# Kernel tuning notes

Measured on AMD Instinct MI355X. Metric: run time of the kernel, lower is better.

Reference implementation:

```python
import jax, jax.numpy as jnp
import numpy as np

HD = 36      # hard-coded per-head dim in the module
TOPK = 16
EPS = 1e-6


def _adaln(h, emb, w, b):
    # w: (2*D, E) torch-layout Linear weight, b: (2*D,)
    eo = jax.nn.silu(emb) @ w.T + b            # (B, 2D)
    scale, shift = jnp.split(eo, 2, axis=-1)   # (B, D) each
    mu = jnp.mean(h, axis=-1, keepdims=True)
    var = jnp.var(h, axis=-1, keepdims=True)   # biased var, matches torch LayerNorm
    hn = (h - mu) / jnp.sqrt(var + EPS)
    return hn * (1.0 + scale[:, None]) + shift[:, None]


def setup_inputs() -> dict:
    B, T, D, E, N, H = 4, 512, 512, 512, 4096, 8
    key = jax.random.key(0)
    ks = jax.random.split(key, 18)
    s = 0.02
    f32 = jnp.float32
    return {
        "x1": jax.random.normal(ks[0], (B, T, D), f32),
        "x2": jax.random.normal(ks[1], (B, T, D), f32),
        "x3": jax.random.normal(ks[2], (B, T, D), f32),
        "xf": jax.random.normal(ks[3], (B, N, D), f32),
        "emb": jax.random.normal(ks[4], (B, E), f32),
        "u_noise": jax.random.uniform(ks[5], (B, H, 3 * T, N // H), f32),
        # AdaLN modulation Linear per branch (zero-init in source; use small random to exercise math)
        "adaln_w": jax.random.normal(ks[6], (3, 2 * D, E), f32) * s,
        "adaln_b": jnp.zeros((3, 2 * D), f32),
        "xfn_w": jax.random.normal(ks[7], (2 * D, E), f32) * s,
        "xfn_b": jnp.zeros((2 * D,), f32),
        "q_w": jax.random.normal(ks[8], (3, H * HD, D), f32) * s,
        "q_b": jnp.zeros((3, H * HD), f32),
        "k_w": jax.random.normal(ks[9], (H, HD, D), f32) * s,
        "k_b": jnp.zeros((H, HD), f32),
        "v_w": jax.random.normal(ks[10], (H, HD, D), f32) * s,
        "v_b": jnp.zeros((H, HD), f32),
        "out_w": jax.random.normal(ks[11], (3, D, H * HD), f32) * s,
        "out_b": jnp.zeros((3, D), f32),
    }


def reference(x1, x2, x3, xf, emb, u_noise, adaln_w, adaln_b, xfn_w, xfn_b,
              q_w, q_b, k_w, k_b, v_w, v_b, out_w, out_b):
    B = x1.shape[0]
    H = k_w.shape[0]
    N = xf.shape[1]
    nh = N // H
    Ts = (x1.shape[1], x2.shape[1], x3.shape[1])

    Qs = []
    for i, x in enumerate((x1, x2, x3)):
        xn = _adaln(x, emb, adaln_w[i], adaln_b[i])
        q = xn @ q_w[i].T + q_b[i]                               # (B,Ti,H*HD)
        Qs.append(q.reshape(B, x.shape[1], H, HD).transpose(0, 2, 1, 3))
    Q = jnp.concatenate(Qs, axis=2)                               # (B,H,T,HD)

    xfn = _adaln(xf, emb, xfn_w, xfn_b).reshape(B, H, nh, -1)     # (B,H,nh,D)
    K = jnp.einsum('bhnd,hkd->bhnk', xfn, k_w) + k_b[:, None, :]  # (B,H,nh,HD)
    V = jnp.einsum('bhnd,hkd->bhnk', xfn, v_w) + v_b[:, None, :]

    logits = jnp.einsum('bhtk,bhnk->bhtn', Q, K) / jnp.sqrt(jnp.float32(HD))
    gumbel = -jnp.log(-jnp.log(u_noise + 1e-9) + 1e-9)
    logits = logits + gumbel                                      # (B,H,T,nh)

    soft = jax.nn.softmax(logits, axis=-1)
    idx = jax.lax.top_k(logits, TOPK)[1]                          # (B,H,T,K)
    mask = jnp.put_along_axis(jnp.zeros_like(logits), idx, 1.0, axis=-1, inplace=False)
    hard = jax.nn.softmax(jnp.where(mask == 0, -jnp.inf, logits), axis=-1)
    attn = hard + soft - jax.lax.stop_gradient(soft)              # straight-through

    out = jnp.einsum('bhtn,bhnk->bhtk', attn, V)                  # (B,H,T,HD)
    out = out.transpose(0, 2, 1, 3).reshape(B, sum(Ts), H * HD)

    o1 = out[:, :Ts[0]] @ out_w[0].T + out_b[0]
    o2 = out[:, Ts[0]:Ts[0] + Ts[1]] @ out_w[1].T + out_b[1]
    o3 = out[:, Ts[0] + Ts[1]:] @ out_w[2].T + out_b[2]
    return (o1, o2, o3)
```

## Files before the change

### kernel.cpp

```cpp
#include <hip/hip_runtime.h>
#include <math.h>

#define FI4(p) (*(const float4*)(p))

typedef _Float16 half8 __attribute__((ext_vector_type(8)));
typedef _Float16 half2v __attribute__((ext_vector_type(2)));
typedef float f32x4 __attribute__((ext_vector_type(4)));

__device__ __forceinline__ float gumbelf(float u) {
    return -__logf(-__logf(u + 1e-9f) + 1e-9f);
}

template<int CTRL>
__device__ __forceinline__ int dppmov(int v) {
    return __builtin_amdgcn_update_dpp(v, v, CTRL, 0xF, 0xF, false);
}
__device__ __forceinline__ float wave_max_bcast(float v) {
    v = fmaxf(v, __int_as_float(dppmov<0xB1>(__float_as_int(v))));
    v = fmaxf(v, __int_as_float(dppmov<0x4E>(__float_as_int(v))));
    v = fmaxf(v, __int_as_float(dppmov<0x141>(__float_as_int(v))));
    v = fmaxf(v, __int_as_float(dppmov<0x140>(__float_as_int(v))));
    v = fmaxf(v, __int_as_float(dppmov<0x142>(__float_as_int(v))));
    v = fmaxf(v, __int_as_float(dppmov<0x143>(__float_as_int(v))));
    return __int_as_float(__builtin_amdgcn_readlane(__float_as_int(v), 63));
}
__device__ __forceinline__ float wave_sum_bcast(float v) {
    v += __int_as_float(dppmov<0xB1>(__float_as_int(v)));
    v += __int_as_float(dppmov<0x4E>(__float_as_int(v)));
    v += __int_as_float(dppmov<0x141>(__float_as_int(v)));
    v += __int_as_float(dppmov<0x140>(__float_as_int(v)));
    v += __int_as_float(dppmov<0x142>(__float_as_int(v)));
    v += __int_as_float(dppmov<0x143>(__float_as_int(v)));
    return __int_as_float(__builtin_amdgcn_readlane(__float_as_int(v), 63));
}

__device__ __forceinline__ unsigned ordkey(float f) {
    unsigned x = __float_as_uint(f);
    return x ^ ((unsigned)((int)x >> 31) | 0x80000000u);
}

__device__ __forceinline__ int mbcnt64(unsigned long long m) {
    return __builtin_amdgcn_mbcnt_hi((unsigned)(m >> 32),
           __builtin_amdgcn_mbcnt_lo((unsigned)m, 0));
}

__device__ __forceinline__ void copy8(unsigned long long* dst, const unsigned long long* src) {
    #pragma unroll
    for (int j = 0; j < 8; ++j) dst[j] = src[j];
}

__device__ __forceinline__ void tie_fill(const unsigned* u, unsigned long long* sel, unsigned hi)
{
    unsigned long long eq[8];
    int mcnt = 0;
    #pragma unroll
    for (int j = 0; j < 8; ++j) {
        sel[j] = __ballot(u[j] > hi);
        eq[j]  = __ballot(u[j] == hi);
        mcnt += __popcll(sel[j]);
    }
    int r = 16 - mcnt;
    #pragma unroll
    for (int jhi = 0; jhi < 2; ++jhi) {
        if (r > 0) {
            unsigned long long any = eq[jhi*4] | eq[jhi*4+1] | eq[jhi*4+2] | eq[jhi*4+3];
            while (any && r > 0) {
                int lane = (int)__builtin_ctzll(any); any &= any - 1;
                #pragma unroll
                for (int jlo = 0; jlo < 4; ++jlo) {
                    int j2 = jhi * 4 + jlo;
                    if (r > 0 && ((eq[j2] >> lane) & 1ull)) { sel[j2] |= 1ull << lane; --r; }
                }
            }
        }
    }
}

__device__ __forceinline__ void select16_pair(
    const unsigned* uA, const unsigned* uB,
    unsigned long long* selA, unsigned long long* selB,
    unsigned loA, unsigned hiA, unsigned loB, unsigned hiB)
{
    bool doneA = false, doneB = false;
    {
        unsigned long long mmA[8], mmB[8];
        int cA = 0, cB = 0;
        #pragma unroll
        for (int j = 0; j < 8; ++j) {
            mmA[j] = __ballot(uA[j] > loA); cA += __popcll(mmA[j]);
            mmB[j] = __ballot(uB[j] > loB); cB += __popcll(mmB[j]);
        }
        if (cA == 16) { copy8(selA, mmA); doneA = true; }
        else if (cA < 16) loA = 0u;
        if (cB == 16) { copy8(selB, mmB); doneB = true; }
        else if (cB < 16) loB = 0u;
    }
    while ((!doneA && hiA - loA > 1u) || (!doneB && hiB - loB > 1u)) {
        bool pA = !doneA && (hiA - loA > 1u);
        bool pB = !doneB && (hiB - loB > 1u);
        unsigned midA = loA + ((hiA - loA) >> 1);
        unsigned midB = loB + ((hiB - loB) >> 1);
        unsigned long long mmA[8], mmB[8];
        int cA = 0, cB = 0;
        #pragma unroll
        for (int j = 0; j < 8; ++j) {
            mmA[j] = __ballot(uA[j] > midA); cA += __popcll(mmA[j]);
            mmB[j] = __ballot(uB[j] > midB); cB += __popcll(mmB[j]);
        }
        if (pA) {
            if (cA == 16) { copy8(selA, mmA); doneA = true; }
            else if (cA > 16) loA = midA; else hiA = midA;
        }
        if (pB) {
            if (cB == 16) { copy8(selB, mmB); doneB = true; }
            else if (cB > 16) loB = midB; else hiB = midB;
        }
    }
    if (!doneA) tie_fill(uA, selA, hiA);
    if (!doneB) tie_fill(uB, selB, hiB);
}

__global__ __launch_bounds__(256) void prep_kernel(
    const float* __restrict__ q_w, const float* __restrict__ k_w,
    const float* __restrict__ v_w, const float* __restrict__ out_w,
    const float* __restrict__ emb,
    const float* __restrict__ adaln_w, const float* __restrict__ adaln_b,
    const float* __restrict__ xfn_w,  const float* __restrict__ xfn_b,
    _Float16* __restrict__ qwh, _Float16* __restrict__ qwl,
    _Float16* __restrict__ kwh, _Float16* __restrict__ kwl,
    _Float16* __restrict__ vw16, _Float16* __restrict__ ow16,
    float* __restrict__ eo)
{
    if (blockIdx.x < 4608) {
        int idx = blockIdx.x * 256 + threadIdx.x;
        if (idx < 442368) {
            float x = q_w[idx];
            _Float16 hi = (_Float16)x;
            qwh[idx] = hi; qwl[idx] = (_Float16)(x - (float)hi);
        } else if (idx < 442368 + 147456) {
            int i = idx - 442368;
            float x = k_w[i];
            _Float16 hi = (_Float16)x;
            kwh[i] = hi; kwl[i] = (_Float16)(x - (float)hi);
        } else if (idx < 442368 + 294912) {
            int i = idx - 442368 - 147456;
            vw16[i] = (_Float16)v_w[i];
        } else {
            int i = idx - 442368 - 294912;
            ow16[i] = (_Float16)out_w[i];
        }
    } else {
        int wid  = (blockIdx.x - 4608) * 4 + (threadIdx.x >> 6);
        int lane = threadIdx.x & 63;
        int l = wid >> 12;
        int rem = wid & 4095;
        int b = rem >> 10;
        int o = rem & 1023;
        const float* wrow = (l < 3) ? (adaln_w + ((size_t)(l * 1024 + o)) * 512)
                                    : (xfn_w + (size_t)o * 512);
        const float* erow = emb + b * 512;
        float acc = 0.f;
        for (int d = lane; d < 512; d += 64) {
            float e = erow[d];
            float se = e / (1.f + __expf(-e));
            acc = fmaf(se, wrow[d], acc);
        }
        #pragma unroll
        for (int off = 32; off; off >>= 1) acc += __shfl_xor(acc, off, 64);
        if (lane == 0) {
            float bias = (l < 3) ? adaln_b[l * 1024 + o] : xfn_b[o];
            eo[wid] = acc + bias;
        }
    }
}

__global__ __launch_bounds__(256) void ln_kernel(
    const float* __restrict__ x1, const float* __restrict__ x2,
    const float* __restrict__ x3, const float* __restrict__ xf,
    const float* __restrict__ eo,
    _Float16* __restrict__ xnqh, _Float16* __restrict__ xnql,
    _Float16* __restrict__ xfnh, _Float16* __restrict__ xfnl)
{
    int row = blockIdx.x;
    const float* src; const float* eorow; _Float16* dh; _Float16* dl;
    if (row < 6144) {
        int l = row >> 11, idx = row & 2047, b = idx >> 9;
        const float* xp = (l == 0) ? x1 : (l == 1) ? x2 : x3;
        src = xp + (size_t)idx * 512;
        eorow = eo + (size_t)(l * 4 + b) * 1024;
        dh = xnqh + (size_t)row * 512;
        dl = xnql + (size_t)row * 512;
    } else {
        int rr = row - 6144; int b = rr >> 12;
        src = xf + (size_t)rr * 512;
        eorow = eo + (size_t)(12 + b) * 1024;
        dh = xfnh + (size_t)rr * 512;
        dl = xfnl + (size_t)rr * 512;
    }
    int tid = threadIdx.x;
    float2 vv = *(const float2*)(src + 2 * tid);
    float s = vv.x + vv.y;
    float q = fmaf(vv.x, vv.x, vv.y * vv.y);
    #pragma unroll
    for (int off = 32; off; off >>= 1) {
        s += __shfl_xor(s, off, 64);
        q += __shfl_xor(q, off, 64);
    }
    __shared__ float red[8];
    int wv = tid >> 6, lane = tid & 63;
    if (lane == 0) { red[wv] = s; red[4 + wv] = q; }
    __syncthreads();
    s = red[0] + red[1] + red[2] + red[3];
    q = red[4] + red[5] + red[6] + red[7];
    float mu  = s * (1.f / 512.f);
    float var = q * (1.f / 512.f) - mu * mu;
    float rs  = 1.f / sqrtf(var + 1e-6f);
    float2 sc = *(const float2*)(eorow + 2 * tid);
    float2 sh = *(const float2*)(eorow + 512 + 2 * tid);
    float r0 = (vv.x - mu) * rs * (1.f + sc.x) + sh.x;
    float r1 = (vv.y - mu) * rs * (1.f + sc.y) + sh.y;
    _Float16 h0 = (_Float16)r0, h1 = (_Float16)r1;
    half2v H = {h0, h1};
    half2v L = {(_Float16)(r0 - (float)h0), (_Float16)(r1 - (float)h1)};
    *(half2v*)(dh + 2 * tid) = H;
    *(half2v*)(dl + 2 * tid) = L;
}

template<int NF, int MODE>
__device__ __forceinline__ void gemm16_body(
    int gw, int l,
    const _Float16* __restrict__ Ah, const _Float16* __restrict__ Al,
    const _Float16* __restrict__ Wh, const _Float16* __restrict__ Wl,
    const float* __restrict__ bias,
    float* __restrict__ O0)
{
    constexpr bool SPLIT = (MODE == 0 || MODE == 1);
    const int Kd = (MODE == 3) ? 288 : 512;
    const int NT = (MODE == 0) ? 6 : (MODE == 3) ? 8 : 1;
    const int mt = gw / NT, nt = gw - mt * NT;
    const int row0 = mt * 32;
    const int col0 = nt * (NF * 16);
    const int lr = l & 15, lk = (l >> 4) * 8;

    int lsel = 0, h = 0;
    if (MODE == 0)                   { lsel = row0 >> 11; }
    else if (MODE == 1 || MODE == 2) { h = (row0 >> 9) & 7; }
    else                             { lsel = row0 >> 11; }

    size_t arow0;
    if (MODE == 3) {
        int rb = row0 & 2047, bb = rb >> 9, t0 = rb & 511;
        arow0 = (size_t)bb * 1536 + (size_t)lsel * 512 + t0;
    } else {
        arow0 = (size_t)row0;
    }

    const _Float16* aph = Ah + (arow0 + lr) * Kd + lk;
    const _Float16* apl = SPLIT ? (Al + (arow0 + lr) * Kd + lk) : nullptr;

    const _Float16* bph[NF];
    const _Float16* bpl[NF];
    #pragma unroll
    for (int f = 0; f < NF; ++f) {
        int c = col0 + f * 16 + lr;
        int wr;
        if (MODE == 0)      wr = lsel * 288 + c;
        else if (MODE == 3) wr = lsel * 512 + c;
        else                wr = h * 36 + (c < 36 ? c : 0);
        bph[f] = Wh + (size_t)wr * Kd + lk;
        if (SPLIT) bpl[f] = Wl + (size_t)wr * Kd + lk;
    }

    f32x4 acc[2][NF];
    #pragma unroll
    for (int mi = 0; mi < 2; ++mi)
        #pragma unroll
        for (int f = 0; f < NF; ++f) acc[mi][f] = (f32x4){0.f, 0.f, 0.f, 0.f};

    for (int kk = 0; kk < Kd; kk += 32) {
        half8 a0h = *(const half8*)(aph + kk);
        half8 a1h = *(const half8*)(aph + (size_t)16 * Kd + kk);
        half8 a0l, a1l;
        if constexpr (SPLIT) {
            a0l = *(const half8*)(apl + kk);
            a1l = *(const half8*)(apl + (size_t)16 * Kd + kk);
        }
        #pragma unroll
        for (int f = 0; f < NF; ++f) {
            half8 bh_ = *(const half8*)(bph[f] + kk);
            acc[0][f] = __builtin_amdgcn_mfma_f32_16x16x32_f16(a0h, bh_, acc[0][f], 0, 0, 0);
            acc[1][f] = __builtin_amdgcn_mfma_f32_16x16x32_f16(a1h, bh_, acc[1][f], 0, 0, 0);
            if constexpr (SPLIT) {
                half8 bl_ = *(const half8*)(bpl[f] + kk);
                acc[0][f] = __builtin_amdgcn_mfma_f32_16x16x32_f16(a0h, bl_, acc[0][f], 0, 0, 0);
                acc[1][f] = __builtin_amdgcn_mfma_f32_16x16x32_f16(a1h, bl_, acc[1][f], 0, 0, 0);
                acc[0][f] = __builtin_amdgcn_mfma_f32_16x16x32_f16(a0l, bh_, acc[0][f], 0, 0, 0);
                acc[1][f] = __builtin_amdgcn_mfma_f32_16x16x32_f16(a1l, bh_, acc[1][f], 0, 0, 0);
            }
        }
    }

    #pragma unroll
    for (int mi = 0; mi < 2; ++mi) {
        int rbase = row0 + mi * 16 + (l >> 4) * 4;
        #pragma unroll
        for (int f = 0; f < NF; ++f) {
            int c = col0 + f * 16 + (l & 15);
            if (MODE == 0) {
                int hh = c / 36, hd = c - hh * 36;
                float bz = bias[lsel * 288 + c];
                #pragma unroll
                for (int j = 0; j < 4; ++j) {
                    int r = rbase + j;
                    int rb = r & 2047, bb2 = rb >> 9, t = rb & 511;
                    O0[(((size_t)bb2 * 8 + hh) * 1536 + lsel * 512 + t) * 36 + hd]
                        = acc[mi][f][j] + bz;
                }
            } else if (MODE == 1) {
                if (c < 36) {
                    int bb2 = row0 >> 12;
                    int n0 = rbase & 511;
                    float bz = bias[h * 36 + c];
                    float4 v4;
                    v4.x = acc[mi][f][0] + bz; v4.y = acc[mi][f][1] + bz;
                    v4.z = acc[mi][f][2] + bz; v4.w = acc[mi][f][3] + bz;
                    *(float4*)&O0[(((size_t)bb2 * 8 + h) * 36 + c) * 512 + n0] = v4;
                }
            } else if (MODE == 2) {
                if (c < 36) {
                    int bb2 = row0 >> 12;
                    int n0 = rbase & 511;
                    float bz = bias[h * 36 + c];
                    #pragma unroll
                    for (int j = 0; j < 4; ++j)
                        O0[(((size_t)bb2 * 8 + h) * 512 + n0 + j) * 36 + c]
                            = acc[mi][f][j] + bz;
                }
            } else {
                float bz = bias[lsel * 512 + c];
                #pragma unroll
                for (int j = 0; j < 4; ++j) {
                    int r = rbase + j;
                    int rb = r & 2047, bb2 = rb >> 9, t = rb & 511;
                    O0[(size_t)lsel * 1048576 + ((size_t)bb2 * 512 + t) * 512 + c]
                        = acc[mi][f][j] + bz;
                }
            }
        }
    }
}

__global__ __launch_bounds__(256) void qkv_kernel(
    const _Float16* __restrict__ xnqh, const _Float16* __restrict__ xnql,
    const _Float16* __restrict__ xfnh, const _Float16* __restrict__ xfnl,
    const _Float16* __restrict__ qwh,  const _Float16* __restrict__ qwl,
    const _Float16* __restrict__ kwh,  const _Float16* __restrict__ kwl,
    const _Float16* __restrict__ vw16,
    const float* __restrict__ q_b, const float* __restrict__ k_b,
    const float* __restrict__ v_b,
    float* __restrict__ Qb, float* __restrict__ Kt, float* __restrict__ Vb)
{
    const int l = threadIdx.x & 63;
    const int w = threadIdx.x >> 6;
    if (blockIdx.x < 288)
        gemm16_body<3, 0>(blockIdx.x * 4 + w, l, xnqh, xnql, qwh, qwl, q_b, Qb);
    else if (blockIdx.x < 416)
        gemm16_body<3, 1>((blockIdx.x - 288) * 4 + w, l, xfnh, xfnl, kwh, kwl, k_b, Kt);
    else
        gemm16_body<3, 2>((blockIdx.x - 416) * 4 + w, l, xfnh, nullptr, vw16, nullptr, v_b, Vb);
}

__global__ __launch_bounds__(256) void outproj_kernel(
    const _Float16* __restrict__ att16, const _Float16* __restrict__ ow16,
    const float* __restrict__ out_b, float* __restrict__ out)
{
    const int l = threadIdx.x & 63;
    const int w = threadIdx.x >> 6;
    gemm16_body<4, 3>(blockIdx.x * 4 + w, l, att16, nullptr, ow16, nullptr, out_b, out);
}

__global__ __launch_bounds__(512, 4) void attn_kernel(
    const float* __restrict__ Qb, const float* __restrict__ Kt,
    const float* __restrict__ Vb, const float* __restrict__ un,
    _Float16* __restrict__ att16)
{
    __shared__ float Q_s[36 * 32];
    __shared__ float CmpW[8][2][2][16];
    __shared__ int   CmpN[8][2][2][16];

    const int tid = threadIdx.x;
    const int bid = ((int)blockIdx.x & 7) * 192 + ((int)blockIdx.x >> 3);
    const int bh = bid / 48;
    const int chunk = bid - bh * 48;
    const int t0p = chunk * 32;
    const int b = bh >> 3, h = bh & 7;
    const int l = tid & 63;
    const int wv = tid >> 6;
    const int w4 = wv * 4;
    const int dpv = l & 31, halfw = l >> 5;
    const float S6 = 1.0f / 6.0f;

    for (int idx = tid; idx < 32 * 36; idx += 512) {
        int r = idx & 31, dd = idx >> 5;
        Q_s[dd * 32 + r] = Qb[((size_t)bh * 1536 + t0p + r) * 36 + dd];
    }
    __syncthreads();

    const float* Ktbh = Kt + (size_t)bh * 18432;
    const float* Vbh  = Vb + (size_t)bh * 18432;

    float acc[4][8];
    #pragma unroll
    for (int r = 0; r < 4; ++r)
        #pragma unroll
        for (int j = 0; j < 8; ++j) acc[r][j] = 0.f;

    #pragma unroll 6
    for (int dd = 0; dd < 36; ++dd) {
        float4 q   = FI4(&Q_s[dd * 32 + w4]);
        const float* ktr = Ktbh + dd * 512;
        float4 ka  = FI4(&ktr[l * 4]);
        float4 kb2 = FI4(&ktr[256 + l * 4]);
        float qv[4] = {q.x, q.y, q.z, q.w};
        float kv[8] = {ka.x, ka.y, ka.z, ka.w, kb2.x, kb2.y, kb2.z, kb2.w};
        #pragma unroll
        for (int r = 0; r < 4; ++r)
            #pragma unroll
            for (int j = 0; j < 8; ++j)
                acc[r][j] = fmaf(qv[r], kv[j], acc[r][j]);
    }

    float4 ub0[4], ub1[4];
    {
        const float* ubase = un + ((size_t)bh * 1536 + t0p + w4) * 512;
        #pragma unroll
        for (int r = 0; r < 4; ++r) {
            ub0[r] = FI4(&ubase[(size_t)r * 512 + l * 4]);
            ub1[r] = FI4(&ubase[(size_t)r * 512 + 256 + l * 4]);
        }
    }

    unsigned key[4][8];
    float m[4];
    #pragma unroll
    for (int r = 0; r < 4; ++r) {
        acc[r][0] = fmaf(acc[r][0], S6, gumbelf(ub0[r].x));
        acc[r][1] = fmaf(acc[r][1], S6, gumbelf(ub0[r].y));
        acc[r][2] = fmaf(acc[r][2], S6, gumbelf(ub0[r].z));
        acc[r][3] = fmaf(acc[r][3], S6, gumbelf(ub0[r].w));
        acc[r][4] = fmaf(acc[r][4], S6, gumbelf(ub1[r].x));
        acc[r][5] = fmaf(acc[r][5], S6, gumbelf(ub1[r].y));
        acc[r][6] = fmaf(acc[r][6], S6, gumbelf(ub1[r].z));
        acc[r][7] = fmaf(acc[r][7], S6, gumbelf(ub1[r].w));
        float mr = acc[r][0];
        #pragma unroll
        for (int j = 0; j < 8; ++j) {
            key[r][j] = ordkey(acc[r][j]);
            mr = fmaxf(mr, acc[r][j]);
        }
        m[r] = wave_max_bcast(mr);
    }

    #pragma unroll
    for (int pr = 0; pr < 2; ++pr) {
        const int rA = pr * 2, rB = pr * 2 + 1;

        unsigned long long selA[8], selB[8];
        select16_pair(key[rA], key[rB], selA, selB,
                      ordkey(m[rA] - 28.0f), ordkey(m[rA]),
                      ordkey(m[rB] - 28.0f), ordkey(m[rB]));

        float psA = 0.f, psB = 0.f;
        {
            int baseA = 0, baseB = 0;
            #pragma unroll
            for (int j = 0; j < 8; ++j) {
                unsigned long long ma = selA[j], mb = selB[j];
                int nj = ((j >> 2) << 8) + l * 4 + (j & 3);
                if ((ma >> l) & 1ull) {
                    float ex = __expf(acc[rA][j] - m[rA]);
                    psA += ex;
                    int rank = baseA + mbcnt64(ma);
                    CmpN[wv][pr][0][rank] = nj;
                    CmpW[wv][pr][0][rank] = ex;
                }
                if ((mb >> l) & 1ull) {
                    float ex = __expf(acc[rB][j] - m[rB]);
                    psB += ex;
                    int rank = baseB + mbcnt64(mb);
                    CmpN[wv][pr][1][rank] = nj;
                    CmpW[wv][pr][1][rank] = ex;
                }
                baseA += __popcll(ma); baseB += __popcll(mb);
            }
        }
        float sumA = wave_sum_bcast(psA);
        float sumB = wave_sum_bcast(psB);
        asm volatile("s_waitcnt lgkmcnt(0)" ::: "memory");

        float od = 0.f, od2 = 0.f;
        #pragma unroll
        for (int k = 0; k < 16; ++k) {
            int nn  = CmpN[wv][pr][halfw][k];
            float w = CmpW[wv][pr][halfw][k];
            const float* vr = Vbh + (size_t)nn * 36;
            od = fmaf(w, vr[dpv], od);
            if (dpv < 4) od2 = fmaf(w, vr[32 + dpv], od2);
        }

        float invs = 1.0f / (halfw ? sumB : sumA);
        int t = t0p + w4 + pr * 2 + halfw;
        _Float16* orow = att16 + ((size_t)b * 1536 + t) * 288 + h * 36;
        orow[dpv] = (_Float16)(od * invs);
        if (dpv < 4) orow[32 + dpv] = (_Float16)(od2 * invs);
    }
}

extern "C" void kernel_launch(void* const* d_in, const int* in_sizes, int n_in,
                              void* d_out, int out_size, void* d_ws, size_t ws_size,
                              hipStream_t stream)
{
    (void)in_sizes; (void)n_in; (void)out_size; (void)ws_size;
    const float* x1      = (const float*)d_in[0];
    const float* x2      = (const float*)d_in[1];
    const float* x3      = (const float*)d_in[2];
    const float* xf      = (const float*)d_in[3];
    const float* emb     = (const float*)d_in[4];
    const float* un      = (const float*)d_in[5];
    const float* adaln_w = (const float*)d_in[6];
    const float* adaln_b = (const float*)d_in[7];
    const float* xfn_w   = (const float*)d_in[8];
    const float* xfn_b   = (const float*)d_in[9];
    const float* q_w     = (const float*)d_in[10];
    const float* q_b     = (const float*)d_in[11];
    const float* k_w     = (const float*)d_in[12];
    const float* k_b     = (const float*)d_in[13];
    const float* v_w     = (const float*)d_in[14];
    const float* v_b     = (const float*)d_in[15];
    const float* out_w   = (const float*)d_in[16];
    const float* out_b   = (const float*)d_in[17];
    float* out = (float*)d_out;

    float* ws = (float*)d_ws;
    float* eo = ws;
    float* Qb = eo + 16384;
    float* Kt = Qb + 1769472;
    float* Vb = Kt + 589824;
    _Float16* xnqh = (_Float16*)(Vb + 589824);
    _Float16* xnql = xnqh + 3145728;
    _Float16* xfnh = xnql + 3145728;
    _Float16* xfnl = xfnh + 8388608;
    _Float16* att16 = xfnl + 8388608;
    _Float16* qwh  = att16 + 1769472;
    _Float16* qwl  = qwh + 442368;
    _Float16* kwh  = qwl + 442368;
    _Float16* kwl  = kwh + 147456;
    _Float16* vw16 = kwl + 147456;
    _Float16* ow16 = vw16 + 147456;

    prep_kernel<<<8704, 256, 0, stream>>>(q_w, k_w, v_w, out_w, emb,
                                          adaln_w, adaln_b, xfn_w, xfn_b,
                                          qwh, qwl, kwh, kwl, vw16, ow16, eo);
    ln_kernel<<<22528, 256, 0, stream>>>(x1, x2, x3, xf, eo, xnqh, xnql, xfnh, xfnl);
    qkv_kernel<<<544, 256, 0, stream>>>(xnqh, xnql, xfnh, xfnl,
                                        qwh, qwl, kwh, kwl, vw16,
                                        q_b, k_b, v_b, Qb, Kt, Vb);
    attn_kernel<<<1536, 512, 0, stream>>>(Qb, Kt, Vb, un, att16);
    outproj_kernel<<<384, 256, 0, stream>>>(att16, ow16, out_b, out);
}
```

Baseline: 183.9 us.

## Compute attention logits with split-fp16 MFMA over padded Q/K layouts

Q and K projections now write split hi/lo fp16 values into row-major buffers padded to 40 columns, with the pad zeroed in the prep kernel. The attention kernel computes the QK^T logits with 16x16x32 f16 MFMAs (three-term hi/lo split) instead of scalar FMAs from LDS-staged Q, stages the scores in a large LDS tile, and reads them back per row. It also tightens the top-k search window from 28 to 8 and lowers the launch-bounds occupancy hint. The aim is to cut the FMA cost of the logit computation, at the price of more LDS use, an extra barrier, and possible precision or selection-window risks.

Result: no change. 182.6 us (-0.7%).

```diff
diff --git a/kernel.cpp b/kernel.cpp
--- a/kernel.cpp
+++ b/kernel.cpp
@@ -129,6 +129,8 @@
     _Float16* __restrict__ qwh, _Float16* __restrict__ qwl,
     _Float16* __restrict__ kwh, _Float16* __restrict__ kwl,
     _Float16* __restrict__ vw16, _Float16* __restrict__ ow16,
+    _Float16* __restrict__ Qph, _Float16* __restrict__ Qpl,
+    _Float16* __restrict__ Kph, _Float16* __restrict__ Kpl,
     float* __restrict__ eo)
 {
     if (blockIdx.x < 4608) {
@@ -149,7 +151,7 @@
             int i = idx - 442368 - 294912;
             ow16[i] = (_Float16)out_w[i];
         }
-    } else {
+    } else if (blockIdx.x < 8704) {
         int wid  = (blockIdx.x - 4608) * 4 + (threadIdx.x >> 6);
         int lane = threadIdx.x & 63;
         int l = wid >> 12;
@@ -170,6 +172,17 @@
         if (lane == 0) {
             float bias = (l < 3) ? adaln_b[l * 1024 + o] : xfn_b[o];
             eo[wid] = acc + bias;
+        }
+    } else {
+        int idx = (blockIdx.x - 8704) * 256 + threadIdx.x;
+        short4 z = {0, 0, 0, 0};
+        if (idx < 49152) {
+            *(short4*)&Qph[(size_t)idx * 40 + 36] = z;
+            *(short4*)&Qpl[(size_t)idx * 40 + 36] = z;
+        } else {
+            int i2 = idx - 49152;
+            *(short4*)&Kph[(size_t)i2 * 40 + 36] = z;
+            *(short4*)&Kpl[(size_t)i2 * 40 + 36] = z;
         }
     }
 }
@@ -232,7 +245,7 @@
     const _Float16* __restrict__ Ah, const _Float16* __restrict__ Al,
     const _Float16* __restrict__ Wh, const _Float16* __restrict__ Wl,
     const float* __restrict__ bias,
-    float* __restrict__ O0)
+    float* __restrict__ Of, _Float16* __restrict__ Oh, _Float16* __restrict__ Ol)
 {
     constexpr bool SPLIT = (MODE == 0 || MODE == 1);
     const int Kd = (MODE == 3) ? 288 : 512;
@@ -313,18 +326,25 @@
                 for (int j = 0; j < 4; ++j) {
                     int r = rbase + j;
                     int rb = r & 2047, bb2 = rb >> 9, t = rb & 511;
-                    O0[(((size_t)bb2 * 8 + hh) * 1536 + lsel * 512 + t) * 36 + hd]
-                        = acc[mi][f][j] + bz;
+                    size_t row = ((size_t)bb2 * 8 + hh) * 1536 + lsel * 512 + t;
+                    float v = acc[mi][f][j] + bz;
+                    _Float16 hi = (_Float16)v;
+                    Oh[row * 40 + hd] = hi;
+                    Ol[row * 40 + hd] = (_Float16)(v - (float)hi);
                 }
             } else if (MODE == 1) {
                 if (c < 36) {
                     int bb2 = row0 >> 12;
                     int n0 = rbase & 511;
                     float bz = bias[h * 36 + c];
-                    float4 v4;
-                    v4.x = acc[mi][f][0] + bz; v4.y = acc[mi][f][1] + bz;
-                    v4.z = acc[mi][f][2] + bz; v4.w = acc[mi][f][3] + bz;
-                    *(float4*)&O0[(((size_t)bb2 * 8 + h) * 36 + c) * 512 + n0] = v4;
+                    #pragma unroll
+                    for (int j = 0; j < 4; ++j) {
+                        size_t row = ((size_t)bb2 * 8 + h) * 512 + n0 + j;
+                        float v = acc[mi][f][j] + bz;
+                        _Float16 hi = (_Float16)v;
+                        Oh[row * 40 + c] = hi;
+                        Ol[row * 40 + c] = (_Float16)(v - (float)hi);
+                    }
                 }
             } else if (MODE == 2) {
                 if (c < 36) {
@@ -333,7 +353,7 @@
                     float bz = bias[h * 36 + c];
                     #pragma unroll
                     for (int j = 0; j < 4; ++j)
-                        O0[(((size_t)bb2 * 8 + h) * 512 + n0 + j) * 36 + c]
+                        Of[(((size_t)bb2 * 8 + h) * 512 + n0 + j) * 36 + c]
                             = acc[mi][f][j] + bz;
                 }
             } else {
@@ -342,7 +362,7 @@
                 for (int j = 0; j < 4; ++j) {
                     int r = rbase + j;
                     int rb = r & 2047, bb2 = rb >> 9, t = rb & 511;
-                    O0[(size_t)lsel * 1048576 + ((size_t)bb2 * 512 + t) * 512 + c]
+                    Of[(size_t)lsel * 1048576 + ((size_t)bb2 * 512 + t) * 512 + c]
                         = acc[mi][f][j] + bz;
                 }
             }
@@ -358,16 +378,21 @@
     const _Float16* __restrict__ vw16,
     const float* __restrict__ q_b, const float* __restrict__ k_b,
     const float* __restrict__ v_b,
-    float* __restrict__ Qb, float* __restrict__ Kt, float* __restrict__ Vb)
+    _Float16* __restrict__ Qph, _Float16* __restrict__ Qpl,
+    _Float16* __restrict__ Kph, _Float16* __restrict__ Kpl,
+    float* __restrict__ Vb)
 {
     const int l = threadIdx.x & 63;
     const int w = threadIdx.x >> 6;
     if (blockIdx.x < 288)
-        gemm16_body<3, 0>(blockIdx.x * 4 + w, l, xnqh, xnql, qwh, qwl, q_b, Qb);
+        gemm16_body<3, 0>(blockIdx.x * 4 + w, l, xnqh, xnql, qwh, qwl, q_b,
+                          nullptr, Qph, Qpl);
     else if (blockIdx.x < 416)
-        gemm16_body<3, 1>((blockIdx.x - 288) * 4 + w, l, xfnh, xfnl, kwh, kwl, k_b, Kt);
+        gemm16_body<3, 1>((blockIdx.x - 288) * 4 + w, l, xfnh, xfnl, kwh, kwl, k_b,
+                          nullptr, Kph, Kpl);
     else
-        gemm16_body<3, 2>((blockIdx.x - 416) * 4 + w, l, xfnh, nullptr, vw16, nullptr, v_b, Vb);
+        gemm16_body<3, 2>((blockIdx.x - 416) * 4 + w, l, xfnh, nullptr, vw16, nullptr, v_b,
+                          Vb, nullptr, nullptr);
 }
 
 __global__ __launch_bounds__(256) void outproj_kernel(
@@ -376,15 +401,17 @@
 {
     const int l = threadIdx.x & 63;
     const int w = threadIdx.x >> 6;
-    gemm16_body<4, 3>(blockIdx.x * 4 + w, l, att16, nullptr, ow16, nullptr, out_b, out);
-}
-
-__global__ __launch_bounds__(512, 4) void attn_kernel(
-    const float* __restrict__ Qb, const float* __restrict__ Kt,
+    gemm16_body<4, 3>(blockIdx.x * 4 + w, l, att16, nullptr, ow16, nullptr, out_b,
+                      out, nullptr, nullptr);
+}
+
+__global__ __launch_bounds__(512, 2) void attn_kernel(
+    const _Float16* __restrict__ Qph, const _Float16* __restrict__ Qpl,
+    const _Float16* __restrict__ Kph, const _Float16* __restrict__ Kpl,
     const float* __restrict__ Vb, const float* __restrict__ un,
     _Float16* __restrict__ att16)
 {
-    __shared__ float Q_s[36 * 32];
+    __shared__ float S_lds[32 * 516];
     __shared__ float CmpW[8][2][2][16];
     __shared__ int   CmpN[8][2][2][16];
 
@@ -399,35 +426,78 @@
     const int w4 = wv * 4;
     const int dpv = l & 31, halfw = l >> 5;
     const float S6 = 1.0f / 6.0f;
-
-    for (int idx = tid; idx < 32 * 36; idx += 512) {
-        int r = idx & 31, dd = idx >> 5;
-        Q_s[dd * 32 + r] = Qb[((size_t)bh * 1536 + t0p + r) * 36 + dd];
-    }
-    __syncthreads();
-
-    const float* Ktbh = Kt + (size_t)bh * 18432;
-    const float* Vbh  = Vb + (size_t)bh * 18432;
-
-    float acc[4][8];
-    #pragma unroll
-    for (int r = 0; r < 4; ++r)
-        #pragma unroll
-        for (int j = 0; j < 8; ++j) acc[r][j] = 0.f;
-
-    #pragma unroll 6
-    for (int dd = 0; dd < 36; ++dd) {
-        float4 q   = FI4(&Q_s[dd * 32 + w4]);
-        const float* ktr = Ktbh + dd * 512;
-        float4 ka  = FI4(&ktr[l * 4]);
-        float4 kb2 = FI4(&ktr[256 + l * 4]);
-        float qv[4] = {q.x, q.y, q.z, q.w};
-        float kv[8] = {ka.x, ka.y, ka.z, ka.w, kb2.x, kb2.y, kb2.z, kb2.w};
-        #pragma unroll
-        for (int r = 0; r < 4; ++r)
-            #pragma unroll
-            for (int j = 0; j < 8; ++j)
-                acc[r][j] = fmaf(qv[r], kv[j], acc[r][j]);
+    const int lr = l & 15, grp = l >> 4;
+
+    {
+        const int n0 = wv * 64;
+        const _Float16* kh = Kph + ((size_t)bh * 512 + n0 + lr) * 40;
+        const _Float16* kl = Kpl + ((size_t)bh * 512 + n0 + lr) * 40;
+        const _Float16* qh = Qph + ((size_t)bh * 1536 + t0p + lr) * 40;
+        const _Float16* ql = Qpl + ((size_t)bh * 1536 + t0p + lr) * 40;
+
+        f32x4 acc[4][2];
+        #pragma unroll
+        for (int mt = 0; mt < 4; ++mt) {
+            acc[mt][0] = (f32x4){0.f, 0.f, 0.f, 0.f};
+            acc[mt][1] = (f32x4){0.f, 0.f, 0.f, 0.f};
+        }
+
+        {
+            const int doff = grp * 8;
+            half8 ah[4], al[4], bh8[2], bl8[2];
+            #pragma unroll
+            for (int mt = 0; mt < 4; ++mt) {
+                ah[mt] = *(const half8*)(kh + (size_t)mt * 640 + doff);
+                al[mt] = *(const half8*)(kl + (size_t)mt * 640 + doff);
+            }
+            #pragma unroll
+            for (int nt = 0; nt < 2; ++nt) {
+                bh8[nt] = *(const half8*)(qh + (size_t)nt * 640 + doff);
+                bl8[nt] = *(const half8*)(ql + (size_t)nt * 640 + doff);
+            }
+            #pragma unroll
+            for (int mt = 0; mt < 4; ++mt)
+                #pragma unroll
+                for (int nt = 0; nt < 2; ++nt) {
+                    acc[mt][nt] = __builtin_amdgcn_mfma_f32_16x16x32_f16(ah[mt], bh8[nt], acc[mt][nt], 0, 0, 0);
+                    acc[mt][nt] = __builtin_amdgcn_mfma_f32_16x16x32_f16(ah[mt], bl8[nt], acc[mt][nt], 0, 0, 0);
+                    acc[mt][nt] = __builtin_amdgcn_mfma_f32_16x16x32_f16(al[mt], bh8[nt], acc[mt][nt], 0, 0, 0);
+                }
+        }
+        {
+            half8 zz = {0, 0, 0, 0, 0, 0, 0, 0};
+            half8 ah[4], al[4], bh8[2], bl8[2];
+            bool has = (grp == 0);
+            #pragma unroll
+            for (int mt = 0; mt < 4; ++mt) {
+                ah[mt] = has ? *(const half8*)(kh + (size_t)mt * 640 + 32) : zz;
+                al[mt] = has ? *(const half8*)(kl + (size_t)mt * 640 + 32) : zz;
+            }
+            #pragma unroll
+            for (int nt = 0; nt < 2; ++nt) {
+                bh8[nt] = has ? *(const half8*)(qh + (size_t)nt * 640 + 32) : zz;
+                bl8[nt] = has ? *(const half8*)(ql + (size_t)nt * 640 + 32) : zz;
+            }
+            #pragma unroll
+            for (int mt = 0; mt < 4; ++mt)
+                #pragma unroll
+                for (int nt = 0; nt < 2; ++nt) {
+                    acc[mt][nt] = __builtin_amdgcn_mfma_f32_16x16x32_f16(ah[mt], bh8[nt], acc[mt][nt], 0, 0, 0);
+                    acc[mt][nt] = __builtin_amdgcn_mfma_f32_16x16x32_f16(ah[mt], bl8[nt], acc[mt][nt], 0, 0, 0);
+                    acc[mt][nt] = __builtin_amdgcn_mfma_f32_16x16x32_f16(al[mt], bh8[nt], acc[mt][nt], 0, 0, 0);
+                }
+        }
+        #pragma unroll
+        for (int mt = 0; mt < 4; ++mt)
+            #pragma unroll
+            for (int nt = 0; nt < 2; ++nt) {
+                int tl = nt * 16 + lr;
+                int nb = n0 + mt * 16 + grp * 4;
+                float4 v;
+                v.x = acc[mt][nt][0] * S6; v.y = acc[mt][nt][1] * S6;
+                v.z = acc[mt][nt][2] * S6; v.w = acc[mt][nt][3] * S6;
+                *(float4*)&S_lds[tl * 516 + nb] = v;
+            }
     }
 
     float4 ub0[4], ub1[4];
@@ -439,19 +509,23 @@
             ub1[r] = FI4(&ubase[(size_t)r * 512 + 256 + l * 4]);
         }
     }
-
+    __syncthreads();
+
+    float acc[4][8];
     unsigned key[4][8];
     float m[4];
     #pragma unroll
     for (int r = 0; r < 4; ++r) {
-        acc[r][0] = fmaf(acc[r][0], S6, gumbelf(ub0[r].x));
-        acc[r][1] = fmaf(acc[r][1], S6, gumbelf(ub0[r].y));
-        acc[r][2] = fmaf(acc[r][2], S6, gumbelf(ub0[r].z));
-        acc[r][3] = fmaf(acc[r][3], S6, gumbelf(ub0[r].w));
-        acc[r][4] = fmaf(acc[r][4], S6, gumbelf(ub1[r].x));
-        acc[r][5] = fmaf(acc[r][5], S6, gumbelf(ub1[r].y));
-        acc[r][6] = fmaf(acc[r][6], S6, gumbelf(ub1[r].z));
-        acc[r][7] = fmaf(acc[r][7], S6, gumbelf(ub1[r].w));
+        float4 s0 = FI4(&S_lds[(w4 + r) * 516 + l * 4]);
+        float4 s1 = FI4(&S_lds[(w4 + r) * 516 + 256 + l * 4]);
+        acc[r][0] = s0.x + gumbelf(ub0[r].x);
+        acc[r][1] = s0.y + gumbelf(ub0[r].y);
+        acc[r][2] = s0.z + gumbelf(ub0[r].z);
+        acc[r][3] = s0.w + gumbelf(ub0[r].w);
+        acc[r][4] = s1.x + gumbelf(ub1[r].x);
+        acc[r][5] = s1.y + gumbelf(ub1[r].y);
+        acc[r][6] = s1.z + gumbelf(ub1[r].z);
+        acc[r][7] = s1.w + gumbelf(ub1[r].w);
         float mr = acc[r][0];
         #pragma unroll
         for (int j = 0; j < 8; ++j) {
@@ -467,8 +541,8 @@
 
         unsigned long long selA[8], selB[8];
         select16_pair(key[rA], key[rB], selA, selB,
-                      ordkey(m[rA] - 28.0f), ordkey(m[rA]),
-                      ordkey(m[rB] - 28.0f), ordkey(m[rB]));
+                      ordkey(m[rA] - 8.0f), ordkey(m[rA]),
+                      ordkey(m[rB] - 8.0f), ordkey(m[rB]));
 
         float psA = 0.f, psB = 0.f;
         {
@@ -498,6 +572,7 @@
         float sumB = wave_sum_bcast(psB);
         asm volatile("s_waitcnt lgkmcnt(0)" ::: "memory");
 
+        const float* Vbh = Vb + (size_t)bh * 18432;
         float od = 0.f, od2 = 0.f;
         #pragma unroll
         for (int k = 0; k < 16; ++k) {
@@ -543,10 +618,12 @@
 
     float* ws = (float*)d_ws;
     float* eo = ws;
-    float* Qb = eo + 16384;
-    float* Kt = Qb + 1769472;
-    float* Vb = Kt + 589824;
-    _Float16* xnqh = (_Float16*)(Vb + 589824);
+    float* Vb = eo + 16384;
+    _Float16* Qph = (_Float16*)(Vb + 589824);
+    _Float16* Qpl = Qph + 1966080;
+    _Float16* Kph = Qpl + 1966080;
+    _Float16* Kpl = Kph + 655360;
+    _Float16* xnqh = Kpl + 655360;
     _Float16* xnql = xnqh + 3145728;
     _Float16* xfnh = xnql + 3145728;
     _Float16* xfnl = xfnh + 8388608;
@@ -558,13 +635,14 @@
     _Float16* vw16 = kwl + 147456;
     _Float16* ow16 = vw16 + 147456;
 
-    prep_kernel<<<8704, 256, 0, stream>>>(q_w, k_w, v_w, out_w, emb,
+    prep_kernel<<<8960, 256, 0, stream>>>(q_w, k_w, v_w, out_w, emb,
                                           adaln_w, adaln_b, xfn_w, xfn_b,
-                                          qwh, qwl, kwh, kwl, vw16, ow16, eo);
+                                          qwh, qwl, kwh, kwl, vw16, ow16,
+                                          Qph, Qpl, Kph, Kpl, eo);
     ln_kernel<<<22528, 256, 0, stream>>>(x1, x2, x3, xf, eo, xnqh, xnql, xfnh, xfnl);
     qkv_kernel<<<544, 256, 0, stream>>>(xnqh, xnql, xfnh, xfnl,
                                         qwh, qwl, kwh, kwl, vw16,
-                                        q_b, k_b, v_b, Qb, Kt, Vb);
-    attn_kernel<<<1536, 512, 0, stream>>>(Qb, Kt, Vb, un, att16);
+                                        q_b, k_b, v_b, Qph, Qpl, Kph, Kpl, Vb);
+    attn_kernel<<<1536, 512, 0, stream>>>(Qph, Qpl, Kph, Kpl, Vb, un, att16);
     outproj_kernel<<<384, 256, 0, stream>>>(att16, ow16, out_b, out);
 }
```
